# Optimization experiments

Measured on AMD Instinct MI355X. Metric: run time of the kernel, lower is better.

## Reference

```python
import jax, jax.numpy as jnp
import numpy as np

NUM_HEADS = 16


def rotate_half(x):
    # '... (j d) -> ... j d' with j=2: split last dim into two halves
    x1, x2 = jnp.split(x, 2, axis=-1)
    return jnp.concatenate([-x2, x1], axis=-1)


def apply_rotary_pos_emb(pos, t):
    # pos: [L, d] broadcast onto t: [B, H, L, d]
    return t * jnp.cos(pos) + rotate_half(t) * jnp.sin(pos)


def setup_inputs() -> dict:
    key = jax.random.key(0)
    ks = jax.random.split(key, 10)
    B, N, KV_N, C = 2, 2048, 2048, 1024
    hd = C // NUM_HEADS
    q = jax.random.normal(ks[0], (B, N, C), dtype=jnp.float32)
    k = jax.random.normal(ks[1], (B, KV_N, C), dtype=jnp.float32)
    v = jax.random.normal(ks[2], (B, KV_N, C), dtype=jnp.float32)
    mask = jax.random.randint(ks[3], (B, KV_N), 0, 2) > 0
    pos_emb = jax.random.normal(ks[4], (KV_N, hd), dtype=jnp.float32)
    s = 1.0 / np.sqrt(C)
    qW = jax.random.normal(ks[5], (C, C), dtype=jnp.float32) * s
    kW = jax.random.normal(ks[6], (C, C), dtype=jnp.float32) * s
    vW = jax.random.normal(ks[7], (C, C), dtype=jnp.float32) * s
    projW = jax.random.normal(ks[8], (C, C), dtype=jnp.float32) * s
    return {"q": q, "k": k, "v": v, "mask": mask, "pos_emb": pos_emb,
            "qW": qW, "kW": kW, "vW": vW, "projW": projW}


def reference(q, k, v, mask, pos_emb, qW, kW, vW, projW):
    B, N, C = q.shape
    H = NUM_HEADS
    hd = C // H
    scale = hd ** -0.5
    # linear projections (no bias)
    q = q @ qW
    k = k @ kW
    v = v @ vW
    # b l (h d) -> b h l d
    split = lambda t: t.reshape(t.shape[0], t.shape[1], H, hd).transpose(0, 2, 1, 3)
    q, k, v = split(q), split(k), split(v)
    q = q * scale
    # inline RoPE on q and k
    q = apply_rotary_pos_emb(pos_emb[:q.shape[-2]], q)
    k = apply_rotary_pos_emb(pos_emb[:k.shape[-2]], k)
    attn = jnp.einsum('bhid,bhjd->bhij', q, k)
    mask_value = -jnp.finfo(attn.dtype).max
    attn = jnp.where(mask[:, None, None, :], attn, mask_value)
    attn = jax.nn.softmax(attn, axis=-1)
    x = jnp.einsum('bhij,bhjd->bhid', attn, v)
    x = x.transpose(0, 2, 1, 3).reshape(B, N, C)
    return x @ projW
```

## Files before the change

### kernel.cpp

```cpp
#include <hip/hip_runtime.h>
#include <hip/hip_bf16.h>

#define BB 2
#define NN 2048
#define KVN 2048
#define CC 1024
#define HH 16
#define HD 64

typedef __bf16 bf16;
typedef __attribute__((ext_vector_type(4))) __bf16 bf16x4;
typedef __attribute__((ext_vector_type(8))) __bf16 bf16x8;
typedef __attribute__((ext_vector_type(4))) float f32x4;

__device__ __forceinline__ void gload_lds16(const void* g, void* l) {
  __builtin_amdgcn_global_load_lds(
      (const __attribute__((address_space(1))) void*)g,
      (__attribute__((address_space(3))) void*)l, 16, 0, 0);
}

__global__ __launch_bounds__(256)
void wtrans(const float* __restrict__ qW, const float* __restrict__ kW,
            const float* __restrict__ vW, const float* __restrict__ pW,
            bf16* __restrict__ Wt) {
  __shared__ bf16 t[64][72];
  const float* in = (blockIdx.z == 0) ? qW : (blockIdx.z == 1) ? kW
                    : (blockIdx.z == 2) ? vW : pW;
  bf16* out = Wt + (size_t)blockIdx.z * CC * CC;
  int r0 = blockIdx.y * 64, c0 = blockIdx.x * 64;
  int tid = threadIdx.x;
  int lr = tid >> 3, lc = (tid & 7) * 8;
  for (int p = 0; p < 2; ++p) {
    int rr = lr + p * 32;
    const float* src = &in[(size_t)(r0 + rr) * CC + c0 + lc];
    float4 a = *(const float4*)src;
    float4 b = *(const float4*)(src + 4);
    t[lc + 0][rr] = (bf16)a.x; t[lc + 1][rr] = (bf16)a.y;
    t[lc + 2][rr] = (bf16)a.z; t[lc + 3][rr] = (bf16)a.w;
    t[lc + 4][rr] = (bf16)b.x; t[lc + 5][rr] = (bf16)b.y;
    t[lc + 6][rr] = (bf16)b.z; t[lc + 7][rr] = (bf16)b.w;
  }
  __syncthreads();
  for (int p = 0; p < 2; ++p) {
    int rr = lr + p * 32;
    *(bf16x8*)&out[(size_t)(c0 + rr) * CC + r0 + lc] = *(const bf16x8*)&t[rr][lc];
  }
}

__global__ __launch_bounds__(256, 3)
void gemm_qkv(const float* __restrict__ qin, const float* __restrict__ kin,
              const float* __restrict__ vin, const bf16* __restrict__ Wt,
              const float* __restrict__ pos, bf16* __restrict__ Qp,
              bf16* __restrict__ Kp, bf16* __restrict__ Vp) {
  __shared__ __align__(16) float Asf[128 * 64];
  __shared__ bf16 Bs[128 * 64];
  const int bid = blockIdx.x;
  const int u = bid & 7, s = bid >> 3;
  const int nblk = s >> 2;
  const int m0 = (u * 4 + (s & 3)) * 128;
  const int z = nblk >> 3;
  const int n0 = (nblk & 7) * 128;
  const float* A = (z == 0) ? qin : (z == 1) ? kin : vin;
  const bf16* Bt = Wt + (size_t)z * CC * CC;
  bf16* Out = (z == 0) ? Qp : (z == 1) ? Kp : Vp;
  const int tid = threadIdx.x;
  const int wave = tid >> 6, lane = tid & 63;
  const int quad = lane >> 4, l15 = lane & 15;
  const int waveM = (wave >> 1) * 64, waveN = (wave & 1) * 64;
  f32x4 acc[4][4] = {};

  for (int k0 = 0; k0 < CC; k0 += 64) {
#pragma unroll
    for (int p = 0; p < 4; ++p) {
      int ch = p * 256 + tid;
      int r = ch >> 3, c = (ch & 7) ^ (r & 7);
      gload_lds16(Bt + (size_t)(n0 + r) * CC + k0 + c * 8, &Bs[ch * 8]);
    }
#pragma unroll
    for (int p = 0; p < 8; ++p) {
      int ch = p * 256 + tid;
      int r = ch >> 4, c = (ch & 15) ^ (r & 15);
      gload_lds16(A + (size_t)(m0 + r) * CC + k0 + c * 4, &Asf[ch * 4]);
    }
    __syncthreads();
    bf16x8 af[4][2], bfr[4][2];
#pragma unroll
    for (int i = 0; i < 4; ++i) {
      int rA = waveM + i * 16 + l15;
      int sw = rA & 15;
      const float* arow = &Asf[rA * 64];
      {
        f32x4 a0 = *(const f32x4*)&arow[(((quad * 2) ^ sw)) * 4];
        f32x4 a1 = *(const f32x4*)&arow[(((quad * 2 + 1) ^ sw)) * 4];
        bf16x8 t;
        t[0] = (bf16)a0[0]; t[1] = (bf16)a0[1]; t[2] = (bf16)a0[2]; t[3] = (bf16)a0[3];
        t[4] = (bf16)a1[0]; t[5] = (bf16)a1[1]; t[6] = (bf16)a1[2]; t[7] = (bf16)a1[3];
        af[i][0] = t;
      }
      {
        f32x4 a2 = *(const f32x4*)&arow[(((quad * 2 + 8) ^ sw)) * 4];
        f32x4 a3 = *(const f32x4*)&arow[(((quad * 2 + 9) ^ sw)) * 4];
        bf16x8 t;
        t[0] = (bf16)a2[0]; t[1] = (bf16)a2[1]; t[2] = (bf16)a2[2]; t[3] = (bf16)a2[3];
        t[4] = (bf16)a3[0]; t[5] = (bf16)a3[1]; t[6] = (bf16)a3[2]; t[7] = (bf16)a3[3];
        af[i][1] = t;
      }
      int rB = waveN + i * 16 + l15;
      bfr[i][0] = *(const bf16x8*)&Bs[(rB * 8 + (quad ^ (rB & 7))) * 8];
      bfr[i][1] = *(const bf16x8*)&Bs[(rB * 8 + ((quad + 4) ^ (rB & 7))) * 8];
    }
#pragma unroll
    for (int mi = 0; mi < 4; ++mi)
#pragma unroll
      for (int ni = 0; ni < 4; ++ni) {
        acc[mi][ni] = __builtin_amdgcn_mfma_f32_16x16x32_bf16(
            af[mi][0], bfr[ni][0], acc[mi][ni], 0, 0, 0);
        acc[mi][ni] = __builtin_amdgcn_mfma_f32_16x16x32_bf16(
            af[mi][1], bfr[ni][1], acc[mi][ni], 0, 0, 0);
      }
    __syncthreads();
  }
  const float scale = (z == 0) ? 0.125f : 1.0f;
#pragma unroll
  for (int mi = 0; mi < 4; ++mi) {
#pragma unroll
    for (int r = 0; r < 4; ++r) {
      int m = m0 + waveM + mi * 16 + quad * 4 + r;
      int l = m & (NN - 1);
      if (z == 2) {
#pragma unroll
        for (int ni = 0; ni < 4; ++ni)
          Out[(size_t)m * CC + n0 + waveN + ni * 16 + l15] = (bf16)acc[mi][ni][r];
      } else {
#pragma unroll
        for (int ni = 0; ni < 2; ++ni) {
          int col = n0 + waveN + ni * 16 + l15;
          int d = ni * 16 + l15;
          float x1 = acc[mi][ni][r], x2 = acc[mi][ni + 2][r];
          float s1, c1, s2f, c2f;
          __sincosf(pos[l * HD + d], &s1, &c1);
          __sincosf(pos[l * HD + d + 32], &s2f, &c2f);
          Out[(size_t)m * CC + col]      = (bf16)((x1 * c1 - x2 * s1) * scale);
          Out[(size_t)m * CC + col + 32] = (bf16)((x2 * c2f + x1 * s2f) * scale);
        }
      }
    }
  }
}

__global__ __launch_bounds__(256)
void kpack_kernel(const bf16* __restrict__ Kp, bf16* __restrict__ Kpack) {
  int tix = blockIdx.x, h = blockIdx.y, b = blockIdx.z;
  int bh = b * HH + h;
#pragma unroll
  for (int p = 0; p < 2; ++p) {
    int sp = p * 256 + threadIdx.x;
    int fs = sp >> 6, lane = sp & 63, quad = (sp >> 4) & 3, l15 = sp & 15;
    int ni = fs >> 1, hf = fs & 1;
    bf16x8 v = *(const bf16x8*)&Kp[((size_t)(b * KVN + tix * 64 + ni * 16 + l15)) * CC
                                   + h * HD + hf * 32 + quad * 8];
    *(bf16x8*)&Kpack[(((size_t)(bh * 32 + tix)) * 8 + fs) * 512 + lane * 8] = v;
  }
}

__global__ __launch_bounds__(256)
void vpack_kernel(const bf16* __restrict__ Vp, const int* __restrict__ mask,
                  bf16* __restrict__ VpA, bf16* __restrict__ VpB) {
  __shared__ bf16 t[64][80];
  int tix = blockIdx.x, h = blockIdx.y, b = blockIdx.z;
  int j0 = tix * 64, bh = b * HH + h;
  const int* maskb = mask + b * KVN;
  int tid = threadIdx.x;
  int lr = tid >> 3, lc = (tid & 7) * 8;
  for (int p = 0; p < 2; ++p) {
    int j = lr + p * 32;
    int mv = maskb[j0 + j];
    bf16x8 v = *(const bf16x8*)&Vp[(size_t)(b * KVN + j0 + j) * CC + h * HD + lc];
#pragma unroll
    for (int uu = 0; uu < 8; ++uu) t[lc + uu][j] = mv ? v[uu] : (bf16)0.f;
  }
  __syncthreads();
  for (int p = 0; p < 3; ++p) {
    int sp = p * 256 + tid;
    if (sp < 640) {
      int fs = sp >> 6, lane = sp & 63, quad = (sp >> 4) & 3, l15 = sp & 15;
      int ni = fs >> 1, hf = fs & 1;
      bf16x8 v;
      if (ni < 4) {
        v = *(const bf16x8*)&t[ni * 16 + l15][hf * 32 + quad * 8];
      } else {
#pragma unroll
        for (int jj = 0; jj < 8; ++jj)
          v[jj] = (l15 == 0) ? (bf16)(float)maskb[j0 + hf * 32 + quad * 8 + jj]
                             : (bf16)0.f;
      }
      bf16* dst = (fs < 6) ? (VpA + (size_t)fs * (1 << 19))
                           : (VpB + (size_t)(fs - 6) * (1 << 19));
      *(bf16x8*)&dst[((size_t)(bh * 32 + tix)) * 512 + lane * 8] = v;
    }
  }
}

__global__ __launch_bounds__(256, 2)
void attn3(const bf16* __restrict__ Qp, const bf16* __restrict__ Kpack,
           const bf16* __restrict__ VpA, const bf16* __restrict__ VpB,
           bf16* __restrict__ X) {
  __shared__ char smem[49152];
  const int tid = threadIdx.x, wave = tid >> 6, lane = tid & 63;
  const int quad = lane >> 4, l15 = lane & 15;
  const int bid = blockIdx.x;
  const int u = bid & 7, s = bid >> 3;
  const int bh = u * 4 + (s & 3), qp = s >> 2;
  const int b = bh >> 4, h = bh & 15;
  const int qc = qp * 2 + (wave >> 1), kh = wave & 1;
  const int q0 = qc * 64;
  const int sw = 2 * (l15 & 7);

  bf16* P = (bf16*)(smem + wave * 2048);
  float* mrg = (float*)(smem + 8192);

  bf16x8 qa[4][2];
#pragma unroll
  for (int g = 0; g < 4; ++g) {
    const bf16* qrow = Qp + ((size_t)(b * NN) + q0 + g * 16 + l15) * CC + h * HD;
    qa[g][0] = *(const bf16x8*)&qrow[quad * 8];
    qa[g][1] = *(const bf16x8*)&qrow[32 + quad * 8];
  }

  f32x4 Oacc[4][5] = {};
  const bf16* kbase = Kpack + (size_t)bh * 32 * 8 * 512;

  for (int it = 0; it < 16; ++it) {
    int t = kh * 16 + it;
    bf16x8 kb[8], vb[10];
#pragma unroll
    for (int fs = 0; fs < 8; ++fs)
      kb[fs] = *(const bf16x8*)&kbase[((size_t)t * 8 + fs) * 512 + lane * 8];
#pragma unroll
    for (int fs = 0; fs < 10; ++fs) {
      const bf16* vbs = (fs < 6) ? (VpA + (size_t)fs * (1 << 19))
                                 : (VpB + (size_t)(fs - 6) * (1 << 19));
      vb[fs] = *(const bf16x8*)&vbs[((size_t)(bh * 32 + t)) * 512 + lane * 8];
    }
#pragma unroll
    for (int g = 0; g < 4; ++g) {
      f32x4 sg[4];
#pragma unroll
      for (int ni = 0; ni < 4; ++ni) {
        f32x4 zz = {};
        zz = __builtin_amdgcn_mfma_f32_16x16x32_bf16(kb[ni * 2], qa[g][0], zz, 0, 0, 0);
        zz = __builtin_amdgcn_mfma_f32_16x16x32_bf16(kb[ni * 2 + 1], qa[g][1], zz, 0, 0, 0);
        sg[ni] = zz;
      }
#pragma unroll
      for (int ni = 0; ni < 4; ++ni) {
        bf16x4 pk;
#pragma unroll
        for (int r = 0; r < 4; ++r) pk[r] = (bf16)__expf(sg[ni][r] - 4.0f);
        *(bf16x4*)&P[(l15 * 16 + ((ni * 4 + quad) ^ sw)) * 4] = pk;
      }
      bf16x8 pf0 = *(const bf16x8*)&P[(l15 * 16 + ((quad * 2) ^ sw)) * 4];
      bf16x8 pf1 = *(const bf16x8*)&P[(l15 * 16 + ((8 + quad * 2) ^ sw)) * 4];
#pragma unroll
      for (int ni = 0; ni < 5; ++ni) {
        Oacc[g][ni] = __builtin_amdgcn_mfma_f32_16x16x32_bf16(vb[ni * 2], pf0, Oacc[g][ni], 0, 0, 0);
        Oacc[g][ni] = __builtin_amdgcn_mfma_f32_16x16x32_bf16(vb[ni * 2 + 1], pf1, Oacc[g][ni], 0, 0, 0);
      }
    }
  }
  if (kh == 1) {
    float* dst = mrg + (wave >> 1) * 5120 + lane * 4;
#pragma unroll
    for (int g = 0; g < 4; ++g)
#pragma unroll
      for (int ni = 0; ni < 5; ++ni)
        *(f32x4*)&dst[(g * 5 + ni) * 256] = Oacc[g][ni];
  }
  __syncthreads();
  if (kh == 0) {
    float* src = mrg + (wave >> 1) * 5120 + lane * 4;
#pragma unroll
    for (int g = 0; g < 4; ++g) {
#pragma unroll
      for (int ni = 0; ni < 5; ++ni) {
        f32x4 o = *(const f32x4*)&src[(g * 5 + ni) * 256];
#pragma unroll
        for (int r = 0; r < 4; ++r) Oacc[g][ni][r] += o[r];
      }
      float ls = __shfl(Oacc[g][4][0], l15, 64);
      float rn = 1.0f / ls;
#pragma unroll
      for (int ni = 0; ni < 4; ++ni) {
        bf16x4 ov;
#pragma unroll
        for (int r = 0; r < 4; ++r) ov[r] = (bf16)(Oacc[g][ni][r] * rn);
        *(bf16x4*)&X[((size_t)(b * NN) + q0 + g * 16 + l15) * CC
                     + h * HD + ni * 16 + quad * 4] = ov;
      }
    }
  }
}

__global__ __launch_bounds__(256, 4)
void gemm_proj(const bf16* __restrict__ A, const bf16* __restrict__ Bt,
               float* __restrict__ Out) {
  __shared__ bf16 As[64 * 64];
  __shared__ bf16 Bs[128 * 64];
  const int bid = blockIdx.x;
  const int u = bid & 7, s = bid >> 3;
  const int m0 = (u * 8 + (s >> 3)) * 64;
  const int n0 = (s & 7) * 128;
  const int tid = threadIdx.x;
  const int wave = tid >> 6, lane = tid & 63;
  const int quad = lane >> 4, l15 = lane & 15;
  const int waveM = (wave >> 1) * 32, waveN = (wave & 1) * 64;
  f32x4 acc[2][4] = {};

  for (int k0 = 0; k0 < CC; k0 += 64) {
#pragma unroll
    for (int p = 0; p < 2; ++p) {
      int ch = p * 256 + tid;
      int r = ch >> 3, c = (ch & 7) ^ (r & 7);
      gload_lds16(A + (size_t)(m0 + r) * CC + k0 + c * 8, &As[ch * 8]);
    }
#pragma unroll
    for (int p = 0; p < 4; ++p) {
      int ch = p * 256 + tid;
      int r = ch >> 3, c = (ch & 7) ^ (r & 7);
      gload_lds16(Bt + (size_t)(n0 + r) * CC + k0 + c * 8, &Bs[ch * 8]);
    }
    __syncthreads();
    bf16x8 af[2][2], bfr[4][2];
#pragma unroll
    for (int i = 0; i < 2; ++i) {
      int rA = waveM + i * 16 + l15;
      af[i][0] = *(const bf16x8*)&As[(rA * 8 + (quad ^ (rA & 7))) * 8];
      af[i][1] = *(const bf16x8*)&As[(rA * 8 + ((quad + 4) ^ (rA & 7))) * 8];
    }
#pragma unroll
    for (int i = 0; i < 4; ++i) {
      int rB = waveN + i * 16 + l15;
      bfr[i][0] = *(const bf16x8*)&Bs[(rB * 8 + (quad ^ (rB & 7))) * 8];
      bfr[i][1] = *(const bf16x8*)&Bs[(rB * 8 + ((quad + 4) ^ (rB & 7))) * 8];
    }
#pragma unroll
    for (int mi = 0; mi < 2; ++mi)
#pragma unroll
      for (int ni = 0; ni < 4; ++ni) {
        acc[mi][ni] = __builtin_amdgcn_mfma_f32_16x16x32_bf16(
            af[mi][0], bfr[ni][0], acc[mi][ni], 0, 0, 0);
        acc[mi][ni] = __builtin_amdgcn_mfma_f32_16x16x32_bf16(
            af[mi][1], bfr[ni][1], acc[mi][ni], 0, 0, 0);
      }
    __syncthreads();
  }
#pragma unroll
  for (int mi = 0; mi < 2; ++mi)
#pragma unroll
    for (int ni = 0; ni < 4; ++ni)
#pragma unroll
      for (int r = 0; r < 4; ++r) {
        int row = m0 + waveM + mi * 16 + quad * 4 + r;
        int col = n0 + waveN + ni * 16 + l15;
        Out[(size_t)row * CC + col] = acc[mi][ni][r];
      }
}

extern "C" void kernel_launch(void* const* d_in, const int* in_sizes, int n_in,
                              void* d_out, int out_size, void* d_ws, size_t ws_size,
                              hipStream_t stream) {
  const float* q    = (const float*)d_in[0];
  const float* k    = (const float*)d_in[1];
  const float* v    = (const float*)d_in[2];
  const int*   mask = (const int*)d_in[3];
  const float* pos  = (const float*)d_in[4];
  const float* qW   = (const float*)d_in[5];
  const float* kW   = (const float*)d_in[6];
  const float* vW   = (const float*)d_in[7];
  const float* pW   = (const float*)d_in[8];
  float* out = (float*)d_out;

  char* w = (char*)d_ws;
  const size_t MB = 1024 * 1024;
  bf16* Wt    = (bf16*)(w);
  bf16* Qp    = (bf16*)(w + 8 * MB);
  bf16* Kp    = (bf16*)(w + 16 * MB);
  bf16* Vp    = (bf16*)(w + 24 * MB);
  bf16* Kpack = (bf16*)(w + 32 * MB);
  bf16* VpA   = (bf16*)(w);
  bf16* VpB   = (bf16*)(w + 40 * MB);
  bf16* X     = (bf16*)(w + 16 * MB);

  wtrans<<<dim3(16, 16, 4), 256, 0, stream>>>(qW, kW, vW, pW, Wt);
  gemm_qkv<<<dim3(768), 256, 0, stream>>>(q, k, v, Wt, pos, Qp, Kp, Vp);
  kpack_kernel<<<dim3(KVN / 64, HH, BB), 256, 0, stream>>>(Kp, Kpack);
  vpack_kernel<<<dim3(KVN / 64, HH, BB), 256, 0, stream>>>(Vp, mask, VpA, VpB);
  attn3<<<dim3(512), 256, 0, stream>>>(Qp, Kpack, VpA, VpB, X);
  gemm_proj<<<dim3(512), 256, 0, stream>>>(X, Wt + 3 * (size_t)CC * CC, out);
}
```

Before: 218.3 us.

## Load fp32 A tiles directly to registers and double-buffer B in LDS

The QKV projection GEMM no longer stages the fp32 activation tile through LDS. Each wave loads its A fragments straight from global memory into registers. The bf16 weight tile is double-buffered in LDS, with the next tile prefetched while the current one is consumed, and only one barrier per iteration. This cuts LDS footprint and traffic and overlaps the weight loads with MFMA work. In exchange, the A global loads now sit on the critical path with vmcnt(0) waits and no prefetch, and A rows are re-read by the two waves that share a waveM.

```diff
diff --git a/kernel.cpp b/kernel.cpp
--- a/kernel.cpp
+++ b/kernel.cpp
@@ -52,8 +52,7 @@
               const float* __restrict__ vin, const bf16* __restrict__ Wt,
               const float* __restrict__ pos, bf16* __restrict__ Qp,
               bf16* __restrict__ Kp, bf16* __restrict__ Vp) {
-  __shared__ __align__(16) float Asf[128 * 64];
-  __shared__ bf16 Bs[128 * 64];
+  __shared__ bf16 Bs[2][128 * 64];
   const int bid = blockIdx.x;
   const int u = bid & 7, s = bid >> 3;
   const int nblk = s >> 2;
@@ -69,45 +68,62 @@
   const int waveM = (wave >> 1) * 64, waveN = (wave & 1) * 64;
   f32x4 acc[4][4] = {};
 
-  for (int k0 = 0; k0 < CC; k0 += 64) {
-#pragma unroll
-    for (int p = 0; p < 4; ++p) {
-      int ch = p * 256 + tid;
-      int r = ch >> 3, c = (ch & 7) ^ (r & 7);
-      gload_lds16(Bt + (size_t)(n0 + r) * CC + k0 + c * 8, &Bs[ch * 8]);
-    }
-#pragma unroll
-    for (int p = 0; p < 8; ++p) {
-      int ch = p * 256 + tid;
-      int r = ch >> 4, c = (ch & 15) ^ (r & 15);
-      gload_lds16(A + (size_t)(m0 + r) * CC + k0 + c * 4, &Asf[ch * 4]);
-    }
-    __syncthreads();
+#pragma unroll
+  for (int p = 0; p < 4; ++p) {
+    int ch = p * 256 + tid;
+    int r = ch >> 3, c = (ch & 7) ^ (r & 7);
+    gload_lds16(Bt + (size_t)(n0 + r) * CC + c * 8, &Bs[0][ch * 8]);
+  }
+
+  int cur = 0;
+  for (int ks = 0; ks < 16; ++ks) {
+    const int k0 = ks * 64;
+    asm volatile("s_waitcnt vmcnt(0)" ::: "memory");
+    __builtin_amdgcn_s_barrier();
+    __builtin_amdgcn_sched_barrier(0);
+
+    f32x4 a0[4], a1[4], a2[4], a3[4];
+#pragma unroll
+    for (int i = 0; i < 4; ++i) {
+      const float* arow =
+          A + (size_t)(m0 + waveM + i * 16 + l15) * CC + k0 + quad * 8;
+      a0[i] = *(const f32x4*)arow;
+      a1[i] = *(const f32x4*)(arow + 4);
+      a2[i] = *(const f32x4*)(arow + 32);
+      a3[i] = *(const f32x4*)(arow + 36);
+    }
+    if (ks < 15) {
+#pragma unroll
+      for (int p = 0; p < 4; ++p) {
+        int ch = p * 256 + tid;
+        int r = ch >> 3, c = (ch & 7) ^ (r & 7);
+        gload_lds16(Bt + (size_t)(n0 + r) * CC + (k0 + 64) + c * 8,
+                    &Bs[cur ^ 1][ch * 8]);
+      }
+    }
+
     bf16x8 af[4][2], bfr[4][2];
 #pragma unroll
     for (int i = 0; i < 4; ++i) {
-      int rA = waveM + i * 16 + l15;
-      int sw = rA & 15;
-      const float* arow = &Asf[rA * 64];
       {
-        f32x4 a0 = *(const f32x4*)&arow[(((quad * 2) ^ sw)) * 4];
-        f32x4 a1 = *(const f32x4*)&arow[(((quad * 2 + 1) ^ sw)) * 4];
         bf16x8 t;
-        t[0] = (bf16)a0[0]; t[1] = (bf16)a0[1]; t[2] = (bf16)a0[2]; t[3] = (bf16)a0[3];
-        t[4] = (bf16)a1[0]; t[5] = (bf16)a1[1]; t[6] = (bf16)a1[2]; t[7] = (bf16)a1[3];
+        t[0] = (bf16)a0[i][0]; t[1] = (bf16)a0[i][1];
+        t[2] = (bf16)a0[i][2]; t[3] = (bf16)a0[i][3];
+        t[4] = (bf16)a1[i][0]; t[5] = (bf16)a1[i][1];
+        t[6] = (bf16)a1[i][2]; t[7] = (bf16)a1[i][3];
         af[i][0] = t;
       }
       {
-        f32x4 a2 = *(const f32x4*)&arow[(((quad * 2 + 8) ^ sw)) * 4];
-        f32x4 a3 = *(const f32x4*)&arow[(((quad * 2 + 9) ^ sw)) * 4];
         bf16x8 t;
-        t[0] = (bf16)a2[0]; t[1] = (bf16)a2[1]; t[2] = (bf16)a2[2]; t[3] = (bf16)a2[3];
-        t[4] = (bf16)a3[0]; t[5] = (bf16)a3[1]; t[6] = (bf16)a3[2]; t[7] = (bf16)a3[3];
+        t[0] = (bf16)a2[i][0]; t[1] = (bf16)a2[i][1];
+        t[2] = (bf16)a2[i][2]; t[3] = (bf16)a2[i][3];
+        t[4] = (bf16)a3[i][0]; t[5] = (bf16)a3[i][1];
+        t[6] = (bf16)a3[i][2]; t[7] = (bf16)a3[i][3];
         af[i][1] = t;
       }
       int rB = waveN + i * 16 + l15;
-      bfr[i][0] = *(const bf16x8*)&Bs[(rB * 8 + (quad ^ (rB & 7))) * 8];
-      bfr[i][1] = *(const bf16x8*)&Bs[(rB * 8 + ((quad + 4) ^ (rB & 7))) * 8];
+      bfr[i][0] = *(const bf16x8*)&Bs[cur][(rB * 8 + (quad ^ (rB & 7))) * 8];
+      bfr[i][1] = *(const bf16x8*)&Bs[cur][(rB * 8 + ((quad + 4) ^ (rB & 7))) * 8];
     }
 #pragma unroll
     for (int mi = 0; mi < 4; ++mi)
@@ -118,7 +134,7 @@
         acc[mi][ni] = __builtin_amdgcn_mfma_f32_16x16x32_bf16(
             af[mi][1], bfr[ni][1], acc[mi][ni], 0, 0, 0);
       }
-    __syncthreads();
+    cur ^= 1;
   }
   const float scale = (z == 0) ? 0.125f : 1.0f;
 #pragma unroll
```

After: 278.7 us. +27.7%, slower.
